# Kernel optimization log

Hardware: AMD Instinct MI355X
Metric: run time of the kernel (lower is better)

The kernel has to match this reference:

```python
import jax, jax.numpy as jnp
import numpy as np

DEGREE = 2
STEPS = 7
N_FEATURES = 120
R_TARGETS = 4
LATENT = 4
D = N_FEATURES + R_TARGETS + LATENT          # 128: padded state dim
N_POLY = 1 + D + D * D                       # 16513: sum_{k=0..degree} D^k for degree=2
BATCH = 16384
W_SCALE = 1e-4                               # keep the iterated quadratic map stable


def setup_inputs() -> dict:
    key = jax.random.key(0)
    k1, k2 = jax.random.split(key)
    X = jax.random.normal(k1, (BATCH, N_FEATURES), dtype=jnp.float32)
    W = jax.random.normal(k2, (N_POLY, D), dtype=jnp.float32) * W_SCALE
    t_init = jnp.zeros((R_TARGETS,), dtype=jnp.float32)
    l_init = jnp.zeros((LATENT,), dtype=jnp.float32)
    return {"X": X, "W": W, "t_init": t_init, "l_init": l_init}


def _poly_full(x):
    """PolynomialFeatures via repeated outer products: [1, x, vec(x xp_{k-1}^T), ...]."""
    n = x.shape[0]
    xp = [jnp.ones((n, 1), x.dtype), x]
    for _ in range(2, DEGREE + 1):
        # [n, D, 1] * [n, 1, P] -> [n, D*P]  (matches tf: X @ expand_dims(XP[-1],1))
        xp.append((x[:, :, None] * xp[-1][:, None, :]).reshape(n, -1))
    return jnp.concatenate(xp, axis=-1)  # [n, N_POLY]


def reference(X, W, t_init, l_init):
    # pad inputs with r_targets + latent_units zeros, then add init values
    inits = jnp.concatenate([jnp.zeros((N_FEATURES,), X.dtype), t_init, l_init])
    x0 = jnp.pad(X, ((0, 0), (0, R_TARGETS + LATENT))) + inits  # [B, D]

    def step(x, _):
        return x + _poly_full(x) @ W, None  # TaylorMap: residual + poly GEMM

    x, _ = jax.lax.scan(step, x0, None, length=STEPS)
    # self._targets = target_features + appended extra target dims
    return x[:, N_FEATURES:N_FEATURES + R_TARGETS]  # [B, n_targets]
```

## Files before the change

### kernel.cpp

```cpp
#include <hip/hip_runtime.h>
#include <hip/hip_bf16.h>


#define DSTATE 128
#define BATCH  16384
#define NSTEPS 7
#define BT     64
#define NSL    585

typedef __attribute__((ext_vector_type(8)))  short  short8;
typedef __attribute__((ext_vector_type(16))) float  f32x16;

__device__ __forceinline__ unsigned short f2bf(float f){
    unsigned int u = __float_as_uint(f);
    u += 0x7fff + ((u >> 16) & 1);
    return (unsigned short)(u >> 16);
}

__global__ void prep_kernel(const float* __restrict__ W, short8* __restrict__ A){
    int gid = blockIdx.x * 256 + threadIdx.x;
    const int ntotal = 4 * 130 * 8 * 64;
    if (gid >= ntotal) return;
    int lane = gid & 63; int r = gid >> 6;
    int s = r & 7;  r >>= 3;
    int row = r % 130;
    int t   = r / 130;
    int d  = t * 32 + (lane & 31);
    int kb = (lane >> 5) * 8;
    int dst;
    bool zero = false;
    if (row < 64){
        int sl = row >> 4;
        if (s < sl) return;
        dst = t * NSL + 9 * row + (s - sl);
    } else if (row < 128){
        int p  = 127 - row;
        int sl = row >> 4;
        if (s < sl) return;
        int ca = 8 - (p >> 4);
        dst = t * NSL + 9 * p + ca + (s - sl);
    } else if (row == 128){
        dst = t * NSL + 576 + s;
    } else {
        if (s) return;
        dst = t * NSL + 584;
        zero = true;
    }
    union { short8 v; unsigned short u[8]; } fr;
#pragma unroll
    for (int e = 0; e < 8; ++e){
        int j = s * 16 + kb + e;
        float v;
        if (zero) v = 0.0f;
        else if (row < 128){
            if      (j < row)  v = 0.0f;
            else if (j == row) v = W[(129 + 128 * row + j) * 128 + d];
            else               v = W[(129 + 128 * row + j) * 128 + d]
                                 + W[(129 + 128 * j + row) * 128 + d];
        } else {
            v = W[(1 + j) * 128 + d];
        }
        fr.u[e] = f2bf(v);
    }
    A[(size_t)dst * 64 + lane] = fr.v;
}

__global__ __launch_bounds__(512)
void taylor_kernel(const float* __restrict__ X, const float* __restrict__ W,
                   const float* __restrict__ tini, const float* __restrict__ lini,
                   const short8* __restrict__ A, float* __restrict__ out)
{
    __shared__ float  x_lds[DSTATE * BT];
    __shared__ float  w0_lds[DSTATE];
    __shared__ short8 bpack[2 * 8 * 64];
    __shared__ float  sc_lds[2][4 * 64 * 17];

    const int tid  = threadIdx.x;
    const int lane = tid & 63;
    const int w    = tid >> 6;
    const int t    = w & 3;
    const int g    = w >> 2;
    const int ln   = lane & 31;
    const int hi   = lane >> 5;
    const int b0   = blockIdx.x * BT;

#pragma unroll
    for (int it = 0; it < 16; ++it){
        int entry = tid + it * 512;
        int b = entry >> 7, d = entry & 127;
        float v;
        if      (d < 120) v = X[(b0 + b) * 120 + d];
        else if (d < 124) v = tini[d - 120];
        else              v = lini[d - 124];
        x_lds[d * BT + b] = v;
    }
    if (tid < DSTATE) w0_lds[tid] = W[tid];

    const short8* const Aw = A + ((size_t)t * NSL + (size_t)g * 288) * 64 + lane;
    const f32x16 zero16 = {};

#pragma unroll 1
    for (int step = 0; step < NSTEPS; ++step){
        __syncthreads();

        const short8* ap = Aw;
        short8 abuf[2][9];
#pragma unroll
        for (int s = 0; s < 9; ++s) abuf[0][s] = ap[s * 64];
        ap += 9 * 64;

#pragma unroll
        for (int f0 = 0; f0 < 2; ++f0){
            int f  = tid + f0 * 512;
            int gg = f >> 9, s = (f >> 6) & 7, l = f & 63;
            int c  = gg * 32 + (l & 31);
            int jb = 16 * s + 8 * (l >> 5);
            union { short8 v; unsigned short u[8]; } fr;
#pragma unroll
            for (int e = 0; e < 8; ++e)
                fr.u[e] = f2bf(x_lds[(jb + e) * BT + c]);
            bpack[f] = fr.v;
        }

        f32x16 acc0, acc1;
        if (g == 0){
#pragma unroll
            for (int r = 0; r < 16; ++r){
                int d = 32 * t + (r & 3) + 8 * (r >> 2) + 4 * hi;
                acc0[r] = x_lds[d * BT + ln]      + w0_lds[d];
                acc1[r] = x_lds[d * BT + 32 + ln] + w0_lds[d];
            }
        } else {
#pragma unroll
            for (int r = 0; r < 16; ++r){ acc0[r] = 0.f; acc1[r] = 0.f; }
        }

        __syncthreads();

#define PAIRS(BK)                                                               \
        _Pragma("unroll 2")                                                     \
        for (int q = 0; q < 16; ++q){                                           \
            const int cur = q & 1, nxt = cur ^ 1;                               \
            _Pragma("unroll")                                                   \
            for (int s = 0; s < 9; ++s) abuf[nxt][s] = ap[s * 64];              \
            ap += 9 * 64;                                                       \
            const int p = 16 * (BK) + q;                                        \
            float s0a = x_lds[p * BT + ln];                                     \
            float s0b = x_lds[p * BT + 32 + ln];                                \
            float s1a = x_lds[(127 - p) * BT + ln];                             \
            float s1b = x_lds[(127 - p) * BT + 32 + ln];                        \
            f32x16 Y0, Y1;                                                      \
            _Pragma("unroll")                                                   \
            for (int s = 0; s < 8 - (BK); ++s){                                 \
                short8 bq0 = bpack[((BK) + s) * 64 + lane];                     \
                short8 bq1 = bpack[512 + ((BK) + s) * 64 + lane];               \
                Y0 = __builtin_amdgcn_mfma_f32_32x32x16_bf16(abuf[cur][s], bq0, s ? Y0 : zero16, 0, 0, 0); \
                Y1 = __builtin_amdgcn_mfma_f32_32x32x16_bf16(abuf[cur][s], bq1, s ? Y1 : zero16, 0, 0, 0); \
            }                                                                   \
            acc0 += s0a * Y0;                                                   \
            acc1 += s0b * Y1;                                                   \
            f32x16 Z0, Z1;                                                      \
            _Pragma("unroll")                                                   \
            for (int s = 0; s < 1 + (BK); ++s){                                 \
                short8 bq0 = bpack[(7 - (BK) + s) * 64 + lane];                 \
                short8 bq1 = bpack[512 + (7 - (BK) + s) * 64 + lane];           \
                Z0 = __builtin_amdgcn_mfma_f32_32x32x16_bf16(abuf[cur][8 - (BK) + s], bq0, s ? Z0 : zero16, 0, 0, 0); \
                Z1 = __builtin_amdgcn_mfma_f32_32x32x16_bf16(abuf[cur][8 - (BK) + s], bq1, s ? Z1 : zero16, 0, 0, 0); \
            }                                                                   \
            acc0 += s1a * Z0;                                                   \
            acc1 += s1b * Z1;                                                   \
        }

        if (g == 0){
            PAIRS(0) PAIRS(1)
        } else {
            PAIRS(2) PAIRS(3)
            f32x16 Y0, Y1;
#pragma unroll
            for (int s = 0; s < 8; ++s){
                short8 bq0 = bpack[s * 64 + lane];
                short8 bq1 = bpack[512 + s * 64 + lane];
                Y0 = __builtin_amdgcn_mfma_f32_32x32x16_bf16(abuf[0][s], bq0, s ? Y0 : zero16, 0, 0, 0);
                Y1 = __builtin_amdgcn_mfma_f32_32x32x16_bf16(abuf[0][s], bq1, s ? Y1 : zero16, 0, 0, 0);
            }
            acc0 += Y0;
            acc1 += Y1;
#pragma unroll
            for (int r = 0; r < 16; ++r){
                sc_lds[0][(t * 64 + lane) * 17 + r] = acc0[r];
                sc_lds[1][(t * 64 + lane) * 17 + r] = acc1[r];
            }
        }
#undef PAIRS

        __syncthreads();
        if (g == 0){
#pragma unroll
            for (int r = 0; r < 16; ++r){
                acc0[r] += sc_lds[0][(t * 64 + lane) * 17 + r];
                acc1[r] += sc_lds[1][(t * 64 + lane) * 17 + r];
            }
            if (step < NSTEPS - 1){
#pragma unroll
                for (int r = 0; r < 16; ++r){
                    int d = 32 * t + (r & 3) + 8 * (r >> 2) + 4 * hi;
                    x_lds[d * BT + ln]      = acc0[r];
                    x_lds[d * BT + 32 + ln] = acc1[r];
                }
            } else if (t == 3 && hi == 0){
                *(float4*)(out + (size_t)(b0 + ln) * 4) =
                    make_float4(acc0[12], acc0[13], acc0[14], acc0[15]);
                *(float4*)(out + (size_t)(b0 + 32 + ln) * 4) =
                    make_float4(acc1[12], acc1[13], acc1[14], acc1[15]);
            }
        }
    }
}

extern "C" void kernel_launch(void* const* d_in, const int* in_sizes, int n_in,
                              void* d_out, int out_size, void* d_ws, size_t ws_size,
                              hipStream_t stream)
{
    const float* X  = (const float*)d_in[0];
    const float* W  = (const float*)d_in[1];
    const float* ti = (const float*)d_in[2];
    const float* li = (const float*)d_in[3];
    float* out      = (float*)d_out;
    short8* A       = (short8*)d_ws;

    const int ntotal = 4 * 130 * 8 * 64;
    prep_kernel<<<(ntotal + 255) / 256, 256, 0, stream>>>(W, A);
    taylor_kernel<<<BATCH / BT, 512, 0, stream>>>(X, W, ti, li, A, out);
}
```

Measured before the change: 366.8 us.

## Hoist B fragments into registers and replace A double-buffer with in-place prefetch

The B operand fragments for each PAIRS block are now loaded once from LDS into registers (bfrag0/bfrag1) and reused across all 16 q iterations, where before they were reloaded from LDS every iteration. The A double buffer is reduced to a single buffer that is refilled slot by slot right after each MFMA consumes it. This cuts LDS traffic and the VGPR cost of double-buffered A, but the extra B fragments add register pressure, and the per-slot refill gives global loads less time to arrive before they are needed.

New measurement: 325.1 us. 11.4% less time.

```diff
diff --git a/kernel.cpp b/kernel.cpp
--- a/kernel.cpp
+++ b/kernel.cpp
@@ -104,9 +104,9 @@
         __syncthreads();
 
         const short8* ap = Aw;
-        short8 abuf[2][9];
-#pragma unroll
-        for (int s = 0; s < 9; ++s) abuf[0][s] = ap[s * 64];
+        short8 abuf[9];
+#pragma unroll
+        for (int s = 0; s < 9; ++s) abuf[s] = ap[s * 64];
         ap += 9 * 64;
 
 #pragma unroll
@@ -137,38 +137,42 @@
 
         __syncthreads();
 
+        short8 bfrag0[8], bfrag1[8];
+
 #define PAIRS(BK)                                                               \
-        _Pragma("unroll 2")                                                     \
-        for (int q = 0; q < 16; ++q){                                           \
-            const int cur = q & 1, nxt = cur ^ 1;                               \
-            _Pragma("unroll")                                                   \
-            for (int s = 0; s < 9; ++s) abuf[nxt][s] = ap[s * 64];              \
-            ap += 9 * 64;                                                       \
-            const int p = 16 * (BK) + q;                                        \
-            float s0a = x_lds[p * BT + ln];                                     \
-            float s0b = x_lds[p * BT + 32 + ln];                                \
-            float s1a = x_lds[(127 - p) * BT + ln];                             \
-            float s1b = x_lds[(127 - p) * BT + 32 + ln];                        \
-            f32x16 Y0, Y1;                                                      \
+        {                                                                       \
             _Pragma("unroll")                                                   \
             for (int s = 0; s < 8 - (BK); ++s){                                 \
-                short8 bq0 = bpack[((BK) + s) * 64 + lane];                     \
-                short8 bq1 = bpack[512 + ((BK) + s) * 64 + lane];               \
-                Y0 = __builtin_amdgcn_mfma_f32_32x32x16_bf16(abuf[cur][s], bq0, s ? Y0 : zero16, 0, 0, 0); \
-                Y1 = __builtin_amdgcn_mfma_f32_32x32x16_bf16(abuf[cur][s], bq1, s ? Y1 : zero16, 0, 0, 0); \
+                bfrag0[s] = bpack[((BK) + s) * 64 + lane];                      \
+                bfrag1[s] = bpack[512 + ((BK) + s) * 64 + lane];                \
             }                                                                   \
-            acc0 += s0a * Y0;                                                   \
-            acc1 += s0b * Y1;                                                   \
-            f32x16 Z0, Z1;                                                      \
-            _Pragma("unroll")                                                   \
-            for (int s = 0; s < 1 + (BK); ++s){                                 \
-                short8 bq0 = bpack[(7 - (BK) + s) * 64 + lane];                 \
-                short8 bq1 = bpack[512 + (7 - (BK) + s) * 64 + lane];           \
-                Z0 = __builtin_amdgcn_mfma_f32_32x32x16_bf16(abuf[cur][8 - (BK) + s], bq0, s ? Z0 : zero16, 0, 0, 0); \
-                Z1 = __builtin_amdgcn_mfma_f32_32x32x16_bf16(abuf[cur][8 - (BK) + s], bq1, s ? Z1 : zero16, 0, 0, 0); \
+            _Pragma("unroll 2")                                                 \
+            for (int q = 0; q < 16; ++q){                                       \
+                const int p = 16 * (BK) + q;                                    \
+                float s0a = x_lds[p * BT + ln];                                 \
+                float s0b = x_lds[p * BT + 32 + ln];                            \
+                float s1a = x_lds[(127 - p) * BT + ln];                         \
+                float s1b = x_lds[(127 - p) * BT + 32 + ln];                    \
+                f32x16 Y0, Y1;                                                  \
+                _Pragma("unroll")                                               \
+                for (int s = 0; s < 8 - (BK); ++s){                             \
+                    Y0 = __builtin_amdgcn_mfma_f32_32x32x16_bf16(abuf[s], bfrag0[s], s ? Y0 : zero16, 0, 0, 0); \
+                    Y1 = __builtin_amdgcn_mfma_f32_32x32x16_bf16(abuf[s], bfrag1[s], s ? Y1 : zero16, 0, 0, 0); \
+                    abuf[s] = ap[s * 64];                                       \
+                }                                                               \
+                acc0 += s0a * Y0;                                               \
+                acc1 += s0b * Y1;                                               \
+                f32x16 Z0, Z1;                                                  \
+                _Pragma("unroll")                                               \
+                for (int s = 0; s < 1 + (BK); ++s){                             \
+                    Z0 = __builtin_amdgcn_mfma_f32_32x32x16_bf16(abuf[8 - (BK) + s], bfrag0[7 - 2 * (BK) + s], s ? Z0 : zero16, 0, 0, 0); \
+                    Z1 = __builtin_amdgcn_mfma_f32_32x32x16_bf16(abuf[8 - (BK) + s], bfrag1[7 - 2 * (BK) + s], s ? Z1 : zero16, 0, 0, 0); \
+                    abuf[8 - (BK) + s] = ap[(8 - (BK) + s) * 64];               \
+                }                                                               \
+                acc0 += s1a * Z0;                                               \
+                acc1 += s1b * Z1;                                               \
+                ap += 9 * 64;                                                   \
             }                                                                   \
-            acc0 += s1a * Z0;                                                   \
-            acc1 += s1b * Z1;                                                   \
         }
 
         if (g == 0){
@@ -178,10 +182,13 @@
             f32x16 Y0, Y1;
 #pragma unroll
             for (int s = 0; s < 8; ++s){
-                short8 bq0 = bpack[s * 64 + lane];
-                short8 bq1 = bpack[512 + s * 64 + lane];
-                Y0 = __builtin_amdgcn_mfma_f32_32x32x16_bf16(abuf[0][s], bq0, s ? Y0 : zero16, 0, 0, 0);
-                Y1 = __builtin_amdgcn_mfma_f32_32x32x16_bf16(abuf[0][s], bq1, s ? Y1 : zero16, 0, 0, 0);
+                bfrag0[s] = bpack[s * 64 + lane];
+                bfrag1[s] = bpack[512 + s * 64 + lane];
+            }
+#pragma unroll
+            for (int s = 0; s < 8; ++s){
+                Y0 = __builtin_amdgcn_mfma_f32_32x32x16_bf16(abuf[s], bfrag0[s], s ? Y0 : zero16, 0, 0, 0);
+                Y1 = __builtin_amdgcn_mfma_f32_32x32x16_bf16(abuf[s], bfrag1[s], s ? Y1 : zero16, 0, 0, 0);
             }
             acc0 += Y0;
             acc1 += Y1;
```
